# Optimization experiments

Hardware: AMD Instinct MI355X
Metric: run time of the kernel (lower is better)

Reference implementation:

```python
import jax, jax.numpy as jnp
import numpy as np

NUM_ROUTING = 3


def squash(v, axis=-1):
    s2 = jnp.sum(jnp.square(v), axis=axis, keepdims=True)
    scale = s2 / (1.0 + s2) / jnp.sqrt(s2 + 1e-7)
    return scale * v


def setup_inputs() -> dict:
    key = jax.random.key(0)
    k1, k2 = jax.random.split(key)
    B, I, D_in, J, D_out = 64, 2304, 8, 32, 16
    inputs = jax.random.normal(k1, (B, I, D_in), dtype=jnp.float32)
    # keras random_uniform(-1, 1)
    W = jax.random.uniform(k2, (I, J, D_in, D_out), dtype=jnp.float32, minval=-1.0, maxval=1.0)
    b0 = jnp.zeros((I, J), dtype=jnp.float32)
    return {"inputs": inputs, "W": W, "b0": b0}


def reference(inputs, W, b0):
    B = inputs.shape[0]
    I, J = b0.shape
    # u_hat[b,i,j,e] = inputs[b,i,:] @ W[i,j,:,e]  -> [B, I, J, E]
    u_hat = jnp.einsum('bid,ijde->bije', inputs, W)
    b = jnp.broadcast_to(b0[None], (B, I, J))
    V = None
    for it in range(NUM_ROUTING):
        c = jax.nn.softmax(b, axis=-1)                      # [B, I, J]
        S = jnp.einsum('bij,bije->bje', c, u_hat)           # [B, J, E]
        V = squash(S)
        if it != NUM_ROUTING - 1:
            b = b + jnp.einsum('bje,bije->bij', V, u_hat)   # agreement update
    return V
```

## Files before the change

### kernel.cpp

```cpp
#include <hip/hip_runtime.h>

#define I_DIM 2304
#define J_DIM 32
#define D_IN  8
#define E_DIM 16
#define B_DIM 64
#define BJE   (B_DIM * J_DIM * E_DIM)
#define NC7   256
#define CH7   (I_DIM / NC7)
#define TILEW 4096
#define XROW  (CH7 * D_IN)

typedef const __attribute__((address_space(1))) char* gcp_t;
typedef __attribute__((address_space(3)))       char* lcp_t;

template <bool FIRST>
__global__ __launch_bounds__(256, 3) void caps_pass_v14(
    const float* __restrict__ x,
    const float* __restrict__ W,
    const float* __restrict__ b0,
    const float* __restrict__ Vacc,
    float* __restrict__ partial)
{
    const int tid   = threadIdx.x;
    const int wv    = __builtin_amdgcn_readfirstlane(tid >> 6);
    const int lane  = tid & 63;
    const int jj    = lane & 31;
    const int eh    = lane >> 5;
    const int km    = jj & 15;
    const int chunk = blockIdx.x & (NC7 - 1);
    const int qb    = blockIdx.x >> 8;
    const int i0    = chunk * CH7;
    const int bloc0 = wv * 4;
    const int bbase = qb * 16 + bloc0;

    __shared__ float Ws[2][TILEW];
    __shared__ float Xall[16 * XROW];
    __shared__ float B0s[CH7 * J_DIM];

    auto stage = [&](int buf, int itile) {
        const char* wt = (const char*)(W + (size_t)itile * TILEW);
#pragma unroll
        for (int r = 0; r < 4; ++r) {
            const int g    = (wv * 4 + r) * 64 + lane;
            const int srcu = (g & ~31) | ((g & 31) ^ ((g >> 5) & 15));
            __builtin_amdgcn_global_load_lds(
                (gcp_t)(wt + (size_t)srcu * 16),
                (lcp_t)((char*)&Ws[buf][(wv * 4 + r) * 256]),
                16, 0, 0);
        }
    };

    stage(0, i0);
    if (tid < 16 * CH7) {
        const int bl = tid / CH7, ii = tid - bl * CH7;
        const float* xp = x + ((size_t)(qb * 16 + bl) * I_DIM + i0 + ii) * D_IN;
        const float4 a  = *(const float4*)xp;
        const float4 b4 = *(const float4*)(xp + 4);
        float* dq = &Xall[bl * XROW + ii * 8];
        *(float4*)dq = a; *(float4*)(dq + 4) = b4;
    }
    {
        B0s[tid] = b0[(i0 + (tid >> 5)) * J_DIM + (tid & 31)];
        if (tid < CH7 * J_DIM - 256)
            B0s[256 + tid] = b0[(i0 + 8) * J_DIM + tid];
    }

    float vacc[4][8];
    if constexpr (!FIRST) {
#pragma unroll
        for (int bb = 0; bb < 4; ++bb) {
            const float* vp = Vacc + ((size_t)((bbase + bb) * J_DIM + jj)) * E_DIM + eh * 8;
            const float4 v0 = *(const float4*)vp;
            const float4 v1 = *(const float4*)(vp + 4);
            vacc[bb][0]=v0.x; vacc[bb][1]=v0.y; vacc[bb][2]=v0.z; vacc[bb][3]=v0.w;
            vacc[bb][4]=v1.x; vacc[bb][5]=v1.y; vacc[bb][6]=v1.z; vacc[bb][7]=v1.w;
        }
    }

    float Sacc[4][8];
#pragma unroll
    for (int bb = 0; bb < 4; ++bb)
#pragma unroll
        for (int e = 0; e < 8; ++e) Sacc[bb][e] = 0.f;

    __syncthreads();

    int cur = 0;
    for (int ii = 0; ii < CH7; ++ii) {
        if (ii + 1 < CH7) stage(cur ^ 1, i0 + ii + 1);

        const float* wb = &Ws[cur][0];
        const float* xr = &Xall[bloc0 * XROW + ii * 8];

        float uh[4][8];
#pragma unroll
        for (int bb = 0; bb < 4; ++bb)
#pragma unroll
            for (int e = 0; e < 8; ++e) uh[bb][e] = 0.f;

        {
            float4 w[8];
#pragma unroll
            for (int d = 0; d < 4; ++d) {
                const int u0 = (d << 2) | (eh << 1);
                w[2*d]   = *(const float4*)&wb[jj * 128 + (((u0    ) ^ km) << 2)];
                w[2*d+1] = *(const float4*)&wb[jj * 128 + (((u0 | 1) ^ km) << 2)];
            }
            float xq[4][4];
#pragma unroll
            for (int bb = 0; bb < 4; ++bb) {
                const float4 t = *(const float4*)(xr + bb * XROW);
                xq[bb][0]=t.x; xq[bb][1]=t.y; xq[bb][2]=t.z; xq[bb][3]=t.w;
            }
#pragma unroll
            for (int d = 0; d < 4; ++d) {
                const float4 wlo = w[2*d], whi = w[2*d+1];
#pragma unroll
                for (int bb = 0; bb < 4; ++bb) {
                    const float xv = xq[bb][d];
                    uh[bb][0] = fmaf(xv, wlo.x, uh[bb][0]);
                    uh[bb][1] = fmaf(xv, wlo.y, uh[bb][1]);
                    uh[bb][2] = fmaf(xv, wlo.z, uh[bb][2]);
                    uh[bb][3] = fmaf(xv, wlo.w, uh[bb][3]);
                    uh[bb][4] = fmaf(xv, whi.x, uh[bb][4]);
                    uh[bb][5] = fmaf(xv, whi.y, uh[bb][5]);
                    uh[bb][6] = fmaf(xv, whi.z, uh[bb][6]);
                    uh[bb][7] = fmaf(xv, whi.w, uh[bb][7]);
                }
            }
        }
        {
            float4 w[8];
#pragma unroll
            for (int d = 4; d < 8; ++d) {
                const int u0 = (d << 2) | (eh << 1);
                w[2*(d-4)]   = *(const float4*)&wb[jj * 128 + (((u0    ) ^ km) << 2)];
                w[2*(d-4)+1] = *(const float4*)&wb[jj * 128 + (((u0 | 1) ^ km) << 2)];
            }
            float xq[4][4];
#pragma unroll
            for (int bb = 0; bb < 4; ++bb) {
                const float4 t = *(const float4*)(xr + bb * XROW + 4);
                xq[bb][0]=t.x; xq[bb][1]=t.y; xq[bb][2]=t.z; xq[bb][3]=t.w;
            }
#pragma unroll
            for (int d = 0; d < 4; ++d) {
                const float4 wlo = w[2*d], whi = w[2*d+1];
#pragma unroll
                for (int bb = 0; bb < 4; ++bb) {
                    const float xv = xq[bb][d];
                    uh[bb][0] = fmaf(xv, wlo.x, uh[bb][0]);
                    uh[bb][1] = fmaf(xv, wlo.y, uh[bb][1]);
                    uh[bb][2] = fmaf(xv, wlo.z, uh[bb][2]);
                    uh[bb][3] = fmaf(xv, wlo.w, uh[bb][3]);
                    uh[bb][4] = fmaf(xv, whi.x, uh[bb][4]);
                    uh[bb][5] = fmaf(xv, whi.y, uh[bb][5]);
                    uh[bb][6] = fmaf(xv, whi.z, uh[bb][6]);
                    uh[bb][7] = fmaf(xv, whi.w, uh[bb][7]);
                }
            }
        }

        const float b0v = B0s[ii * J_DIM + jj];
#pragma unroll
        for (int bb = 0; bb < 4; ++bb) {
            float l;
            if constexpr (FIRST) {
                l = b0v;
            } else {
                float l0 = 0.f, l1 = 0.f;
#pragma unroll
                for (int e = 0; e < 8; e += 2) {
                    l0 = fmaf(vacc[bb][e],     uh[bb][e],     l0);
                    l1 = fmaf(vacc[bb][e + 1], uh[bb][e + 1], l1);
                }
                float lg = l0 + l1;
                lg += __shfl_xor(lg, 32);
                l = b0v + lg;
            }

            const float p = __expf(l);
            float s = p;
#pragma unroll
            for (int k = 16; k >= 1; k >>= 1) s += __shfl_xor(s, k);
            const float c = p * __builtin_amdgcn_rcpf(s);

#pragma unroll
            for (int e = 0; e < 8; ++e) Sacc[bb][e] = fmaf(c, uh[bb][e], Sacc[bb][e]);
        }

        __syncthreads();
        cur ^= 1;
    }

#pragma unroll
    for (int bb = 0; bb < 4; ++bb) {
        float* pp = partial + (size_t)chunk * BJE
                  + ((size_t)((bbase + bb) * J_DIM + jj)) * E_DIM + eh * 8;
        *(float4*)pp       = make_float4(Sacc[bb][0], Sacc[bb][1], Sacc[bb][2], Sacc[bb][3]);
        *(float4*)(pp + 4) = make_float4(Sacc[bb][4], Sacc[bb][5], Sacc[bb][6], Sacc[bb][7]);
    }
}

__global__ __launch_bounds__(256) void reduce_squash(
    const float* __restrict__ partial, float* __restrict__ Vacc,
    float* __restrict__ out, const int nc, const int first_it, const int final_it)
{
    const int t = blockIdx.x * blockDim.x + threadIdx.x;
    float a0=0.f,a1=0.f,a2=0.f,a3=0.f,a4=0.f,a5=0.f,a6=0.f,a7=0.f;
    for (int c = 0; c < nc; c += 8) {
        a0 += partial[(size_t)(c+0) * BJE + t];
        a1 += partial[(size_t)(c+1) * BJE + t];
        a2 += partial[(size_t)(c+2) * BJE + t];
        a3 += partial[(size_t)(c+3) * BJE + t];
        a4 += partial[(size_t)(c+4) * BJE + t];
        a5 += partial[(size_t)(c+5) * BJE + t];
        a6 += partial[(size_t)(c+6) * BJE + t];
        a7 += partial[(size_t)(c+7) * BJE + t];
    }
    const float acc = ((a0+a1)+(a2+a3)) + ((a4+a5)+(a6+a7));

    float s2 = acc * acc;
#pragma unroll
    for (int k = 8; k >= 1; k >>= 1) s2 += __shfl_xor(s2, k);
    const float scale = s2 / (1.f + s2) * rsqrtf(s2 + 1e-7f);
    const float v = scale * acc;
    if (final_it)      out[t] = v;
    else if (first_it) Vacc[t] = v;
    else               Vacc[t] += v;
}

extern "C" void kernel_launch(void* const* d_in, const int* in_sizes, int n_in,
                              void* d_out, int out_size, void* d_ws, size_t ws_size,
                              hipStream_t stream) {
    const float* x  = (const float*)d_in[0];
    const float* W  = (const float*)d_in[1];
    const float* b0 = (const float*)d_in[2];
    float* out = (float*)d_out;

    float* partial = (float*)d_ws;
    float* Vacc    = partial + (size_t)NC7 * BJE;

    caps_pass_v14<true><<<NC7 * 4, 256, 0, stream>>>(x, W, b0, Vacc, partial);
    reduce_squash<<<BJE / 256, 256, 0, stream>>>(partial, Vacc, out, NC7, 1, 0);

    caps_pass_v14<false><<<NC7 * 4, 256, 0, stream>>>(x, W, b0, Vacc, partial);
    reduce_squash<<<BJE / 256, 256, 0, stream>>>(partial, Vacc, out, NC7, 0, 0);

    caps_pass_v14<false><<<NC7 * 4, 256, 0, stream>>>(x, W, b0, Vacc, partial);
    reduce_squash<<<BJE / 256, 256, 0, stream>>>(partial, Vacc, out, NC7, 0, 1);
}
```

Baseline: 166.4 us.

## Replace double-buffered W tiles with five-slot half-tile ring and fine-grained vmcnt waits

The W staging changes from two full 16KB buffers to a ring of five 8KB half-tiles, with four half-tiles prefetched up front. Each half is consumed as soon as it arrives. The __syncthreads calls are replaced by explicit s_waitcnt vmcnt counts plus raw s_barrier, so loads for later halves stay in flight while the current one is computed. The Vacc loads are moved before staging and drained with vmcnt(0) so the counters stay exact. The risks are fragile hand-tuned wait counts, which must match the global-load issue order, and extra barriers per iteration. LDS use rises slightly (40KB vs 32KB for W), which may affect the three-blocks-per-CU occupancy target.

After: 186.6 us. 1.12x slower.

```diff
diff --git a/kernel.cpp b/kernel.cpp
--- a/kernel.cpp
+++ b/kernel.cpp
@@ -10,12 +10,13 @@
 #define CH7   (I_DIM / NC7)
 #define TILEW 4096
 #define XROW  (CH7 * D_IN)
+#define HWF   2048
 
 typedef const __attribute__((address_space(1))) char* gcp_t;
 typedef __attribute__((address_space(3)))       char* lcp_t;
 
 template <bool FIRST>
-__global__ __launch_bounds__(256, 3) void caps_pass_v14(
+__global__ __launch_bounds__(256, 3) void caps_pass_v15(
     const float* __restrict__ x,
     const float* __restrict__ W,
     const float* __restrict__ b0,
@@ -34,24 +35,43 @@
     const int bloc0 = wv * 4;
     const int bbase = qb * 16 + bloc0;
 
-    __shared__ float Ws[2][TILEW];
+    __shared__ float Wh[5 * HWF];
     __shared__ float Xall[16 * XROW];
     __shared__ float B0s[CH7 * J_DIM];
 
-    auto stage = [&](int buf, int itile) {
-        const char* wt = (const char*)(W + (size_t)itile * TILEW);
-#pragma unroll
-        for (int r = 0; r < 4; ++r) {
-            const int g    = (wv * 4 + r) * 64 + lane;
-            const int srcu = (g & ~31) | ((g & 31) ^ ((g >> 5) & 15));
+    auto stage_half = [&](int buf, int h) {
+        const int tile = h >> 1, p = h & 1;
+        const char* wt = (const char*)(W + (size_t)(i0 + tile) * TILEW);
+        float* dst = &Wh[buf * HWF];
+#pragma unroll
+        for (int r = 0; r < 2; ++r) {
+            const int g = r * 256 + wv * 64 + lane;
+            const int j = g >> 4, u = g & 15;
+            const int srcu = j * 32 + p * 16 + (u ^ (j & 15));
             __builtin_amdgcn_global_load_lds(
                 (gcp_t)(wt + (size_t)srcu * 16),
-                (lcp_t)((char*)&Ws[buf][(wv * 4 + r) * 256]),
+                (lcp_t)((char*)dst + (size_t)(r * 256 + wv * 64) * 16),
                 16, 0, 0);
         }
     };
 
-    stage(0, i0);
+    float vacc[4][8];
+    if constexpr (!FIRST) {
+#pragma unroll
+        for (int bb = 0; bb < 4; ++bb) {
+            const float* vp = Vacc + ((size_t)((bbase + bb) * J_DIM + jj)) * E_DIM + eh * 8;
+            const float4 v0 = *(const float4*)vp;
+            const float4 v1 = *(const float4*)(vp + 4);
+            vacc[bb][0]=v0.x; vacc[bb][1]=v0.y; vacc[bb][2]=v0.z; vacc[bb][3]=v0.w;
+            vacc[bb][4]=v1.x; vacc[bb][5]=v1.y; vacc[bb][6]=v1.z; vacc[bb][7]=v1.w;
+        }
+        asm volatile("s_waitcnt vmcnt(0)" ::: "memory");
+    }
+
+    stage_half(0, 0);
+    stage_half(1, 1);
+    stage_half(2, 2);
+    stage_half(3, 3);
     if (tid < 16 * CH7) {
         const int bl = tid / CH7, ii = tid - bl * CH7;
         const float* xp = x + ((size_t)(qb * 16 + bl) * I_DIM + i0 + ii) * D_IN;
@@ -66,47 +86,28 @@
             B0s[256 + tid] = b0[(i0 + 8) * J_DIM + tid];
     }
 
-    float vacc[4][8];
-    if constexpr (!FIRST) {
-#pragma unroll
-        for (int bb = 0; bb < 4; ++bb) {
-            const float* vp = Vacc + ((size_t)((bbase + bb) * J_DIM + jj)) * E_DIM + eh * 8;
-            const float4 v0 = *(const float4*)vp;
-            const float4 v1 = *(const float4*)(vp + 4);
-            vacc[bb][0]=v0.x; vacc[bb][1]=v0.y; vacc[bb][2]=v0.z; vacc[bb][3]=v0.w;
-            vacc[bb][4]=v1.x; vacc[bb][5]=v1.y; vacc[bb][6]=v1.z; vacc[bb][7]=v1.w;
-        }
-    }
-
     float Sacc[4][8];
 #pragma unroll
     for (int bb = 0; bb < 4; ++bb)
 #pragma unroll
         for (int e = 0; e < 8; ++e) Sacc[bb][e] = 0.f;
 
-    __syncthreads();
-
-    int cur = 0;
+    asm volatile("s_waitcnt vmcnt(6) lgkmcnt(0)" ::: "memory");
+    __builtin_amdgcn_s_barrier();
+
+    int cur = 0, stg = 4;
     for (int ii = 0; ii < CH7; ++ii) {
-        if (ii + 1 < CH7) stage(cur ^ 1, i0 + ii + 1);
-
-        const float* wb = &Ws[cur][0];
+        float uh[4][8];
+#pragma unroll
+        for (int bb = 0; bb < 4; ++bb)
+#pragma unroll
+            for (int e = 0; e < 8; ++e) uh[bb][e] = 0.f;
+
         const float* xr = &Xall[bloc0 * XROW + ii * 8];
 
-        float uh[4][8];
-#pragma unroll
-        for (int bb = 0; bb < 4; ++bb)
-#pragma unroll
-            for (int e = 0; e < 8; ++e) uh[bb][e] = 0.f;
-
+        if (ii < 7) { stage_half(stg, 2 * ii + 4); stg = (stg == 4) ? 0 : stg + 1; }
         {
-            float4 w[8];
-#pragma unroll
-            for (int d = 0; d < 4; ++d) {
-                const int u0 = (d << 2) | (eh << 1);
-                w[2*d]   = *(const float4*)&wb[jj * 128 + (((u0    ) ^ km) << 2)];
-                w[2*d+1] = *(const float4*)&wb[jj * 128 + (((u0 | 1) ^ km) << 2)];
-            }
+            const float* wb = &Wh[cur * HWF];
             float xq[4][4];
 #pragma unroll
             for (int bb = 0; bb < 4; ++bb) {
@@ -115,7 +116,9 @@
             }
 #pragma unroll
             for (int d = 0; d < 4; ++d) {
-                const float4 wlo = w[2*d], whi = w[2*d+1];
+                const int u0 = (d << 2) | (eh << 1);
+                const float4 wlo = *(const float4*)&wb[jj * 64 + (((u0    ) ^ km) << 2)];
+                const float4 whi = *(const float4*)&wb[jj * 64 + (((u0 | 1) ^ km) << 2)];
 #pragma unroll
                 for (int bb = 0; bb < 4; ++bb) {
                     const float xv = xq[bb][d];
@@ -130,14 +133,15 @@
                 }
             }
         }
+        cur = (cur == 4) ? 0 : cur + 1;
+        if (ii < 7)       asm volatile("s_waitcnt vmcnt(6)" ::: "memory");
+        else if (ii == 7) asm volatile("s_waitcnt vmcnt(4)" ::: "memory");
+        else              asm volatile("s_waitcnt vmcnt(0)" ::: "memory");
+        __builtin_amdgcn_s_barrier();
+
+        if (ii < 7) { stage_half(stg, 2 * ii + 5); stg = (stg == 4) ? 0 : stg + 1; }
         {
-            float4 w[8];
-#pragma unroll
-            for (int d = 4; d < 8; ++d) {
-                const int u0 = (d << 2) | (eh << 1);
-                w[2*(d-4)]   = *(const float4*)&wb[jj * 128 + (((u0    ) ^ km) << 2)];
-                w[2*(d-4)+1] = *(const float4*)&wb[jj * 128 + (((u0 | 1) ^ km) << 2)];
-            }
+            const float* wb = &Wh[cur * HWF];
             float xq[4][4];
 #pragma unroll
             for (int bb = 0; bb < 4; ++bb) {
@@ -146,7 +150,9 @@
             }
 #pragma unroll
             for (int d = 0; d < 4; ++d) {
-                const float4 wlo = w[2*d], whi = w[2*d+1];
+                const int u0 = (d << 2) | (eh << 1);
+                const float4 wlo = *(const float4*)&wb[jj * 64 + (((u0    ) ^ km) << 2)];
+                const float4 whi = *(const float4*)&wb[jj * 64 + (((u0 | 1) ^ km) << 2)];
 #pragma unroll
                 for (int bb = 0; bb < 4; ++bb) {
                     const float xv = xq[bb][d];
@@ -161,6 +167,7 @@
                 }
             }
         }
+        cur = (cur == 4) ? 0 : cur + 1;
 
         const float b0v = B0s[ii * J_DIM + jj];
 #pragma unroll
@@ -179,19 +186,22 @@
                 lg += __shfl_xor(lg, 32);
                 l = b0v + lg;
             }
-
             const float p = __expf(l);
             float s = p;
 #pragma unroll
             for (int k = 16; k >= 1; k >>= 1) s += __shfl_xor(s, k);
             const float c = p * __builtin_amdgcn_rcpf(s);
-
 #pragma unroll
             for (int e = 0; e < 8; ++e) Sacc[bb][e] = fmaf(c, uh[bb][e], Sacc[bb][e]);
         }
 
-        __syncthreads();
-        cur ^= 1;
+        if (ii < 7) {
+            asm volatile("s_waitcnt vmcnt(6)" ::: "memory");
+            __builtin_amdgcn_s_barrier();
+        } else if (ii == 7) {
+            asm volatile("s_waitcnt vmcnt(2)" ::: "memory");
+            __builtin_amdgcn_s_barrier();
+        }
     }
 
 #pragma unroll
@@ -242,12 +252,12 @@
     float* partial = (float*)d_ws;
     float* Vacc    = partial + (size_t)NC7 * BJE;
 
-    caps_pass_v14<true><<<NC7 * 4, 256, 0, stream>>>(x, W, b0, Vacc, partial);
+    caps_pass_v15<true><<<NC7 * 4, 256, 0, stream>>>(x, W, b0, Vacc, partial);
     reduce_squash<<<BJE / 256, 256, 0, stream>>>(partial, Vacc, out, NC7, 1, 0);
 
-    caps_pass_v14<false><<<NC7 * 4, 256, 0, stream>>>(x, W, b0, Vacc, partial);
+    caps_pass_v15<false><<<NC7 * 4, 256, 0, stream>>>(x, W, b0, Vacc, partial);
     reduce_squash<<<BJE / 256, 256, 0, stream>>>(partial, Vacc, out, NC7, 0, 0);
 
-    caps_pass_v14<false><<<NC7 * 4, 256, 0, stream>>>(x, W, b0, Vacc, partial);
+    caps_pass_v15<false><<<NC7 * 4, 256, 0, stream>>>(x, W, b0, Vacc, partial);
     reduce_squash<<<BJE / 256, 256, 0, stream>>>(partial, Vacc, out, NC7, 0, 1);
 }
```
